# Optimization experiments

Measured on AMD Instinct MI355X. Metric: run time of the kernel, lower is better.

The kernel has to match this reference:

```python
import jax, jax.numpy as jnp
import numpy as np

B, T, C = 4, 2048, 1024
H = 16
D = C // H  # head_dim = 64


def setup_inputs() -> dict:
    key = jax.random.key(0)
    k1, k2, k3 = jax.random.split(key, 3)
    x = jax.random.normal(k1, (B, T, C), dtype=jnp.float32)
    w_qkv = jax.random.normal(k2, (C, 3 * C), dtype=jnp.float32) * (1.0 / np.sqrt(C))
    b_qkv = jnp.zeros((3 * C,), dtype=jnp.float32)
    w_out = jax.random.normal(k3, (C, C), dtype=jnp.float32) * (1.0 / np.sqrt(C))
    b_out = jnp.zeros((C,), dtype=jnp.float32)
    return {"x": x, "w_qkv": w_qkv, "b_qkv": b_qkv, "w_out": w_out, "b_out": b_out}


def reference(x, w_qkv, b_qkv, w_out, b_out):
    # QKV projection: [B,T,3C]
    qkv = x @ w_qkv + b_qkv
    q, k, v = jnp.split(qkv, 3, axis=-1)
    # [B,H,T,D]
    q = q.reshape(B, T, H, D).transpose(0, 2, 1, 3)
    k = k.reshape(B, T, H, D).transpose(0, 2, 1, 3)
    v = v.reshape(B, T, H, D).transpose(0, 2, 1, 3)
    scale = 1.0 / np.sqrt(D)
    # scores: [B,H,T,T]
    scores = jnp.einsum("bhqd,bhkd->bhqk", q, k) * scale
    causal = jnp.tril(jnp.ones((T, T), dtype=bool))
    scores = jnp.where(causal[None, None, :, :], scores, -jnp.inf)
    attn = jax.nn.softmax(scores, axis=-1)
    out = jnp.einsum("bhqk,bhkd->bhqd", attn, v)
    out = out.transpose(0, 2, 1, 3).reshape(B, T, C)
    return out @ w_out + b_out
```

## Files before the change

kernel.cpp:

```cpp
#include <hip/hip_runtime.h>
#include <hip/hip_bf16.h>

#define BB 4
#define TT 2048
#define CC 1024
#define HH 16
#define DD 64

typedef __attribute__((ext_vector_type(8))) short short8;
typedef __attribute__((ext_vector_type(4))) float f32x4;

__device__ __forceinline__ float bf2f(short s) {
  unsigned u = ((unsigned)(unsigned short)s) << 16;
  float f;
  __builtin_memcpy(&f, &u, 4);
  return f;
}
__device__ __forceinline__ short f2bf(float f) {
  unsigned u;
  __builtin_memcpy(&u, &f, 4);
  u = (u + 0x7fffu + ((u >> 16) & 1u)) >> 16;
  return (short)u;
}

__device__ __forceinline__ unsigned cvt_pk_bf16(float lo, float hi) {
  unsigned r;
  asm("v_cvt_pk_bf16_f32 %0, %1, %2" : "=v"(r) : "v"(lo), "v"(hi));
  return r;
}

__device__ __forceinline__ float exp2_fast(float x) {
  float r;
  asm("v_exp_f32 %0, %1" : "=v"(r) : "v"(x));
  return r;
}

template <int CTRL>
__device__ __forceinline__ float dpp_f(float v) {
  union { float f; int i; } u;
  u.f = v;
  u.i = __builtin_amdgcn_update_dpp(0, u.i, CTRL, 0xf, 0xf, true);
  return u.f;
}
__device__ __forceinline__ float rowmax16(float v) {
  v = fmaxf(v, dpp_f<0x128>(v));
  v = fmaxf(v, dpp_f<0x124>(v));
  v = fmaxf(v, dpp_f<0x4E>(v));
  v = fmaxf(v, dpp_f<0xB1>(v));
  return v;
}
__device__ __forceinline__ float rowsum16(float v) {
  v += dpp_f<0x128>(v);
  v += dpp_f<0x124>(v);
  v += dpp_f<0x4E>(v);
  v += dpp_f<0xB1>(v);
  return v;
}

__device__ __forceinline__ void gload_lds16(const void* g, void* l) {
  __builtin_amdgcn_global_load_lds(
      (const __attribute__((address_space(1))) void*)g,
      (__attribute__((address_space(3))) void*)l, 16, 0, 0);
}

__global__ __launch_bounds__(256) void cast_bf16_kernel(
    const float* __restrict__ in, short* __restrict__ out, int n) {
  int i = (blockIdx.x * 256 + threadIdx.x) * 4;
  if (i >= n) return;
  float4 v = *(const float4*)&in[i];
  short4 o;
  o.x = f2bf(v.x); o.y = f2bf(v.y); o.z = f2bf(v.z); o.w = f2bf(v.w);
  *(short4*)&out[i] = o;
}

__global__ __launch_bounds__(256) void transpose_cast_kernel(
    const float* __restrict__ in, short* __restrict__ out, int R, int Cc) {
  __shared__ float tile[32][33];
  const int tx = threadIdx.x, ty = threadIdx.y;
  const int c0 = blockIdx.x * 32, r0 = blockIdx.y * 32;
#pragma unroll
  for (int i = 0; i < 32; i += 8)
    tile[ty + i][tx] = in[(size_t)(r0 + ty + i) * Cc + c0 + tx];
  __syncthreads();
#pragma unroll
  for (int i = 0; i < 32; i += 8)
    out[(size_t)(c0 + ty + i) * R + r0 + tx] = f2bf(tile[tx][ty + i]);
}

template <int MODE>
__global__ __launch_bounds__(256) void gemm_bf16(
    const short* __restrict__ A, const short* __restrict__ Bt,
    const float* __restrict__ bias, float* __restrict__ outF,
    short* __restrict__ outQ, short* __restrict__ outK, short* __restrict__ outV,
    int M, int N, int K) {
  __shared__ __align__(16) short As[128 * 32];
  __shared__ __align__(16) short Bs[128 * 32];
  const int tid = threadIdx.x;
  const int lane = tid & 63, wid = tid >> 6;
  const int wm = wid >> 1, wn = wid & 1;
  const int row0 = blockIdx.y * 128, col0 = blockIdx.x * 128;
  const int fr = lane & 15, fq = lane >> 4;
  const short* Ab = A + (size_t)row0 * K;
  const short* Bb = Bt + (size_t)col0 * K;
  const int sr = tid >> 2;
  const int so = (tid & 3) * 8;

  f32x4 acc[4][4];
#pragma unroll
  for (int m = 0; m < 4; ++m)
#pragma unroll
    for (int n = 0; n < 4; ++n) {
      f32x4 z = {0.f, 0.f, 0.f, 0.f};
      acc[m][n] = z;
    }

  for (int k0 = 0; k0 < K; k0 += 32) {
    __syncthreads();
    gload_lds16(Ab + (size_t)sr * K + k0 + so, &As[tid * 8]);
    gload_lds16(Ab + (size_t)(sr + 64) * K + k0 + so, &As[2048 + tid * 8]);
    gload_lds16(Bb + (size_t)sr * K + k0 + so, &Bs[tid * 8]);
    gload_lds16(Bb + (size_t)(sr + 64) * K + k0 + so, &Bs[2048 + tid * 8]);
    __syncthreads();
    short8 a[4], b[4];
#pragma unroll
    for (int m = 0; m < 4; ++m)
      a[m] = *(const short8*)&As[(wm * 64 + m * 16 + fr) * 32 + fq * 8];
#pragma unroll
    for (int n = 0; n < 4; ++n)
      b[n] = *(const short8*)&Bs[(wn * 64 + n * 16 + fr) * 32 + fq * 8];
#pragma unroll
    for (int m = 0; m < 4; ++m)
#pragma unroll
      for (int n = 0; n < 4; ++n)
        acc[m][n] = __builtin_amdgcn_mfma_f32_16x16x32_bf16(a[m], b[n], acc[m][n], 0, 0, 0);
  }

  float bv[4];
#pragma unroll
  for (int n = 0; n < 4; ++n) bv[n] = bias[col0 + wn * 64 + n * 16 + fr];

  if (MODE == 0) {
#pragma unroll
    for (int m = 0; m < 4; ++m) {
      const int grow = row0 + wm * 64 + m * 16 + fq * 4;
#pragma unroll
      for (int n = 0; n < 4; ++n) {
        const int gcol = col0 + wn * 64 + n * 16 + fr;
#pragma unroll
        for (int r = 0; r < 4; ++r)
          outF[(size_t)(grow + r) * N + gcol] = acc[m][n][r] + bv[n];
      }
    }
  } else {
#pragma unroll
    for (int n = 0; n < 4; ++n) {
      const int gcol = col0 + wn * 64 + n * 16 + fr;
      const int which = gcol >> 10;
      const int h = (gcol & 1023) >> 6;
      const int d = gcol & 63;
      short* dst = (which == 0) ? outQ : (which == 1) ? outK : outV;
#pragma unroll
      for (int m = 0; m < 4; ++m) {
        const int grow = row0 + wm * 64 + m * 16 + fq * 4;
#pragma unroll
        for (int r = 0; r < 4; ++r) {
          const int gb = (grow + r) >> 11;
          const int gt = (grow + r) & 2047;
          const int bh = gb * HH + h;
          size_t idx;
          if (which == 2)
            idx = ((size_t)bh * DD + d) * TT + gt;
          else
            idx = ((size_t)bh * TT + gt) * DD + d;
          dst[idx] = f2bf(acc[m][n][r] + bv[n]);
        }
      }
    }
  }
}

#define C2 0.18033688f

__global__ __launch_bounds__(256) void attn_mfma_kernel(
    const short* __restrict__ q,
    const short* __restrict__ k,
    const short* __restrict__ vt,
    short* __restrict__ ctx) {
  __shared__ __align__(16) short Ks[2][128 * 64];
  __shared__ __align__(16) short Vs[2][64 * 128];
  __shared__ __align__(16) short Ps[4][32 * 64];
  const int tid = threadIdx.x, lane = tid & 63, wid = tid >> 6;
  const int fr = lane & 15, fq = lane >> 4;
  const int lin = blockIdx.x;
  const int bh = lin & 63;
  const int qt = 15 - (lin >> 6);
  const int q0 = qt * 128;
  const int qw0 = q0 + wid * 32;
  const short* kbp = k + (size_t)bh * TT * DD;
  const short* vbp = vt + (size_t)bh * DD * TT;
  char* PsB = (char*)&Ps[wid][0];

#define KSB(c) ((char*)&Ks[0][0] + (c) * (128 * 64 * 2))
#define VSB(c) ((char*)&Vs[0][0] + (c) * (64 * 128 * 2))

  short8 aq[2][2];
#pragma unroll
  for (int m = 0; m < 2; ++m)
#pragma unroll
    for (int ks = 0; ks < 2; ++ks)
      aq[m][ks] = *(const short8*)&q[((size_t)bh * TT + qw0 + m * 16 + fr) * DD + ks * 32 + fq * 8];

  float M[2][4], L[2][4];
  f32x4 o[2][4];
#pragma unroll
  for (int m = 0; m < 2; ++m)
#pragma unroll
    for (int r = 0; r < 4; ++r) { M[m][r] = -1e30f; L[m][r] = 0.f; }
#pragma unroll
  for (int m = 0; m < 2; ++m)
#pragma unroll
    for (int dg = 0; dg < 4; ++dg) {
      f32x4 z = {0.f, 0.f, 0.f, 0.f};
      o[m][dg] = z;
    }

  const int nt = qt + 1;

#define STAGE(c, tt)                                                           \
  do {                                                                         \
    const int kv0_ = (tt) * 128;                                               \
    _Pragma("unroll") for (int b_ = 0; b_ < 4; ++b_) {                         \
      const int lo_ = b_ * 4096 + tid * 16;                                    \
      const int row_ = lo_ >> 7;                                               \
      const int colb_ = lo_ & 127;                                             \
      const int src_ = colb_ ^ ((row_ & 7) << 4);                              \
      gload_lds16(kbp + ((size_t)(kv0_ + row_)) * DD + (src_ >> 1),            \
                  KSB(c) + lo_);                                               \
    }                                                                          \
    _Pragma("unroll") for (int b_ = 0; b_ < 4; ++b_) {                         \
      const int lo_ = b_ * 4096 + tid * 16;                                    \
      const int row_ = lo_ >> 8;                                               \
      const int colb_ = lo_ & 255;                                             \
      const int src_ = colb_ ^ ((row_ & 7) << 4);                              \
      gload_lds16(vbp + (size_t)row_ * TT + kv0_ + (src_ >> 1),                \
                  VSB(c) + lo_);                                               \
    }                                                                          \
  } while (0)

  STAGE(0, 0);

  for (int t = 0; t < nt; ++t) {
    const int cur = t & 1;
    asm volatile("s_waitcnt vmcnt(0)" ::: "memory");
    __builtin_amdgcn_s_barrier();
    if (t + 1 < nt) STAGE(cur ^ 1, t + 1);
    const int kv0 = t * 128;
    if (kv0 > qw0 + 31) continue;

#pragma unroll
    for (int sub = 0; sub < 2; ++sub) {
      const int kv0s = kv0 + sub * 64;
      if (kv0s > qw0 + 31) continue;
      const bool domask = (kv0s + 63 > qw0);

      short8 bk[4][2];
#pragma unroll
      for (int n = 0; n < 4; ++n) {
        const int row = sub * 64 + n * 16 + fr;
#pragma unroll
        for (int ks = 0; ks < 2; ++ks)
          bk[n][ks] = *(const short8*)(KSB(cur) + row * 128 +
                                       (((ks * 64 + fq * 16) ^ ((row & 7) << 4))));
      }
      f32x4 s[2][4];
      __builtin_amdgcn_s_setprio(1);
#pragma unroll
      for (int m = 0; m < 2; ++m)
#pragma unroll
        for (int n = 0; n < 4; ++n) {
          f32x4 z = {0.f, 0.f, 0.f, 0.f};
          s[m][n] = z;
#pragma unroll
          for (int ks = 0; ks < 2; ++ks)
            s[m][n] = __builtin_amdgcn_mfma_f32_16x16x32_bf16(aq[m][ks], bk[n][ks], s[m][n], 0, 0, 0);
        }
      __builtin_amdgcn_s_setprio(0);

      if (domask) {
#pragma unroll
        for (int m = 0; m < 2; ++m)
#pragma unroll
          for (int n = 0; n < 4; ++n)
#pragma unroll
            for (int r = 0; r < 4; ++r) {
              const int qq = qw0 + m * 16 + fq * 4 + r;
              const int kk = kv0s + n * 16 + fr;
              if (kk > qq) s[m][n][r] = -1e30f;
            }
      }

#pragma unroll
      for (int m = 0; m < 2; ++m) {
        float rm2[4];
#pragma unroll
        for (int r = 0; r < 4; ++r) {
          float rm = fmaxf(fmaxf(s[m][0][r], s[m][1][r]), fmaxf(s[m][2][r], s[m][3][r]));
          rm2[r] = rowmax16(rm) * C2;
        }
        float dmax = fmaxf(fmaxf(rm2[0] - M[m][0], rm2[1] - M[m][1]),
                           fmaxf(rm2[2] - M[m][2], rm2[3] - M[m][3]));
        if (__any(dmax > 8.0f)) {
#pragma unroll
          for (int r = 0; r < 4; ++r) {
            const float Mn = fmaxf(M[m][r], rm2[r]);
            const float corr = exp2_fast(M[m][r] - Mn);
            M[m][r] = Mn;
            L[m][r] *= corr;
#pragma unroll
            for (int dg = 0; dg < 4; ++dg) o[m][dg][r] *= corr;
          }
        }
        float psum[4] = {0.f, 0.f, 0.f, 0.f};
        const int brow = m * 16 + fq * 4;
        unsigned short* pw = (unsigned short*)PsB;
#pragma unroll
        for (int n = 0; n < 4; ++n) {
          const float p0 = exp2_fast(__builtin_fmaf(s[m][n][0], C2, -M[m][0]));
          const float p1 = exp2_fast(__builtin_fmaf(s[m][n][1], C2, -M[m][1]));
          const float p2 = exp2_fast(__builtin_fmaf(s[m][n][2], C2, -M[m][2]));
          const float p3 = exp2_fast(__builtin_fmaf(s[m][n][3], C2, -M[m][3]));
          psum[0] += p0; psum[1] += p1; psum[2] += p2; psum[3] += p3;
          const unsigned u0 = cvt_pk_bf16(p0, p1);
          const unsigned u1 = cvt_pk_bf16(p2, p3);
          const int colb = n * 32 + fr * 2;
          pw[((brow + 0) * 128 + (colb ^ (((brow + 0) & 7) << 4))) >> 1] = (unsigned short)u0;
          pw[((brow + 1) * 128 + (colb ^ (((brow + 1) & 7) << 4))) >> 1] = (unsigned short)(u0 >> 16);
          pw[((brow + 2) * 128 + (colb ^ (((brow + 2) & 7) << 4))) >> 1] = (unsigned short)u1;
          pw[((brow + 3) * 128 + (colb ^ (((brow + 3) & 7) << 4))) >> 1] = (unsigned short)(u1 >> 16);
        }
#pragma unroll
        for (int r = 0; r < 4; ++r) L[m][r] += rowsum16(psum[r]);
      }

      short8 ap[2][2], bv[4][2];
#pragma unroll
      for (int m = 0; m < 2; ++m) {
        const int qrow = m * 16 + fr;
#pragma unroll
        for (int ks = 0; ks < 2; ++ks)
          ap[m][ks] = *(const short8*)(PsB + qrow * 128 +
                                       (((ks * 64 + fq * 16) ^ ((qrow & 7) << 4))));
      }
#pragma unroll
      for (int dg = 0; dg < 4; ++dg) {
        const int row = dg * 16 + fr;
#pragma unroll
        for (int ks = 0; ks < 2; ++ks)
          bv[dg][ks] = *(const short8*)(VSB(cur) + row * 256 +
                                        (((sub * 128 + ks * 64 + fq * 16) ^ ((row & 7) << 4))));
      }
      __builtin_amdgcn_s_setprio(1);
#pragma unroll
      for (int m = 0; m < 2; ++m)
#pragma unroll
        for (int dg = 0; dg < 4; ++dg)
#pragma unroll
          for (int ks = 0; ks < 2; ++ks)
            o[m][dg] = __builtin_amdgcn_mfma_f32_16x16x32_bf16(ap[m][ks], bv[dg][ks], o[m][dg], 0, 0, 0);
      __builtin_amdgcn_s_setprio(0);
    }
  }

  const int b = bh >> 4, h = bh & 15;
#pragma unroll
  for (int m = 0; m < 2; ++m)
#pragma unroll
    for (int dg = 0; dg < 4; ++dg)
#pragma unroll
      for (int r = 0; r < 4; ++r) {
        const int qq = qw0 + m * 16 + fq * 4 + r;
        ctx[((size_t)(b * TT + qq)) * CC + h * DD + dg * 16 + fr] =
            f2bf(o[m][dg][r] / L[m][r]);
      }
}

extern "C" void kernel_launch(void* const* d_in, const int* in_sizes, int n_in,
                              void* d_out, int out_size, void* d_ws, size_t ws_size,
                              hipStream_t stream) {
  (void)in_sizes; (void)n_in; (void)out_size; (void)ws_size;
  const float* x = (const float*)d_in[0];
  const float* w_qkv = (const float*)d_in[1];
  const float* b_qkv = (const float*)d_in[2];
  const float* w_out = (const float*)d_in[3];
  const float* b_out = (const float*)d_in[4];
  float* out = (float*)d_out;

  char* w = (char*)d_ws;
  short* xb    = (short*)w; w += (size_t)BB * TT * CC * 2;
  short* wqkvT = (short*)w; w += (size_t)3 * CC * CC * 2;
  short* woutT = (short*)w; w += (size_t)CC * CC * 2;
  short* qb    = (short*)w; w += (size_t)BB * HH * TT * DD * 2;
  short* kb    = (short*)w; w += (size_t)BB * HH * TT * DD * 2;
  short* vtb   = (short*)w; w += (size_t)BB * HH * DD * TT * 2;
  short* ctx   = (short*)w; w += (size_t)BB * TT * CC * 2;

  const int M = BB * TT;

  cast_bf16_kernel<<<dim3((M * CC) / 4 / 256), dim3(256), 0, stream>>>(x, xb, M * CC);
  transpose_cast_kernel<<<dim3(3 * CC / 32, CC / 32), dim3(32, 8), 0, stream>>>(
      w_qkv, wqkvT, CC, 3 * CC);
  transpose_cast_kernel<<<dim3(CC / 32, CC / 32), dim3(32, 8), 0, stream>>>(
      w_out, woutT, CC, CC);

  gemm_bf16<1><<<dim3((3 * CC) / 128, M / 128), dim3(256), 0, stream>>>(
      xb, wqkvT, b_qkv, nullptr, qb, kb, vtb, M, 3 * CC, CC);

  attn_mfma_kernel<<<dim3(16 * 64), dim3(256), 0, stream>>>(qb, kb, vtb, ctx);

  gemm_bf16<0><<<dim3(CC / 128, M / 128), dim3(256), 0, stream>>>(
      ctx, woutT, b_out, out, nullptr, nullptr, nullptr, M, CC, CC);
}
```

Measured before the change: 309.0 us.

## Drop LDS K/V staging; load K and V fragments directly from global per wave

Removes the shared-memory double-buffered K/V staging, its barriers and the block-wide tile loop. Each wave now walks only its own causal range in 64-key steps and loads K and V^T MFMA fragments straight from global memory into registers. This removes block synchronisation and LDS traffic and frees LDS for higher occupancy. In exchange the four waves of a block no longer share K/V reads, so global and L2 traffic rises and load latency is exposed without software pipelining.

```diff
diff --git a/kernel.cpp b/kernel.cpp
--- a/kernel.cpp
+++ b/kernel.cpp
@@ -186,23 +186,17 @@
     const short* __restrict__ k,
     const short* __restrict__ vt,
     short* __restrict__ ctx) {
-  __shared__ __align__(16) short Ks[2][128 * 64];
-  __shared__ __align__(16) short Vs[2][64 * 128];
   __shared__ __align__(16) short Ps[4][32 * 64];
   const int tid = threadIdx.x, lane = tid & 63, wid = tid >> 6;
   const int fr = lane & 15, fq = lane >> 4;
   const int lin = blockIdx.x;
   const int bh = lin & 63;
   const int qt = 15 - (lin >> 6);
-  const int q0 = qt * 128;
-  const int qw0 = q0 + wid * 32;
+  const int qw0 = qt * 128 + wid * 32;
   const short* kbp = k + (size_t)bh * TT * DD;
   const short* vbp = vt + (size_t)bh * DD * TT;
   char* PsB = (char*)&Ps[wid][0];
 
-#define KSB(c) ((char*)&Ks[0][0] + (c) * (128 * 64 * 2))
-#define VSB(c) ((char*)&Vs[0][0] + (c) * (64 * 128 * 2))
-
   short8 aq[2][2];
 #pragma unroll
   for (int m = 0; m < 2; ++m)
@@ -224,151 +218,114 @@
       o[m][dg] = z;
     }
 
-  const int nt = qt + 1;
-
-#define STAGE(c, tt)                                                           \
-  do {                                                                         \
-    const int kv0_ = (tt) * 128;                                               \
-    _Pragma("unroll") for (int b_ = 0; b_ < 4; ++b_) {                         \
-      const int lo_ = b_ * 4096 + tid * 16;                                    \
-      const int row_ = lo_ >> 7;                                               \
-      const int colb_ = lo_ & 127;                                             \
-      const int src_ = colb_ ^ ((row_ & 7) << 4);                              \
-      gload_lds16(kbp + ((size_t)(kv0_ + row_)) * DD + (src_ >> 1),            \
-                  KSB(c) + lo_);                                               \
-    }                                                                          \
-    _Pragma("unroll") for (int b_ = 0; b_ < 4; ++b_) {                         \
-      const int lo_ = b_ * 4096 + tid * 16;                                    \
-      const int row_ = lo_ >> 8;                                               \
-      const int colb_ = lo_ & 255;                                             \
-      const int src_ = colb_ ^ ((row_ & 7) << 4);                              \
-      gload_lds16(vbp + (size_t)row_ * TT + kv0_ + (src_ >> 1),                \
-                  VSB(c) + lo_);                                               \
-    }                                                                          \
-  } while (0)
-
-  STAGE(0, 0);
-
-  for (int t = 0; t < nt; ++t) {
-    const int cur = t & 1;
-    asm volatile("s_waitcnt vmcnt(0)" ::: "memory");
-    __builtin_amdgcn_s_barrier();
-    if (t + 1 < nt) STAGE(cur ^ 1, t + 1);
-    const int kv0 = t * 128;
-    if (kv0 > qw0 + 31) continue;
-
-#pragma unroll
-    for (int sub = 0; sub < 2; ++sub) {
-      const int kv0s = kv0 + sub * 64;
-      if (kv0s > qw0 + 31) continue;
-      const bool domask = (kv0s + 63 > qw0);
-
-      short8 bk[4][2];
+  const int ntw = (qw0 >> 6) + 1;
+
+  for (int t = 0; t < ntw; ++t) {
+    const int kv0s = t * 64;
+    const bool domask = (kv0s + 63 > qw0);
+
+    short8 bk[4][2];
+#pragma unroll
+    for (int n = 0; n < 4; ++n)
+#pragma unroll
+      for (int ks = 0; ks < 2; ++ks)
+        bk[n][ks] = *(const short8*)&kbp[(size_t)(kv0s + n * 16 + fr) * DD + ks * 32 + fq * 8];
+
+    f32x4 s[2][4];
+    __builtin_amdgcn_s_setprio(1);
+#pragma unroll
+    for (int m = 0; m < 2; ++m)
 #pragma unroll
       for (int n = 0; n < 4; ++n) {
-        const int row = sub * 64 + n * 16 + fr;
+        f32x4 z = {0.f, 0.f, 0.f, 0.f};
+        s[m][n] = z;
 #pragma unroll
         for (int ks = 0; ks < 2; ++ks)
-          bk[n][ks] = *(const short8*)(KSB(cur) + row * 128 +
-                                       (((ks * 64 + fq * 16) ^ ((row & 7) << 4))));
-      }
-      f32x4 s[2][4];
-      __builtin_amdgcn_s_setprio(1);
+          s[m][n] = __builtin_amdgcn_mfma_f32_16x16x32_bf16(aq[m][ks], bk[n][ks], s[m][n], 0, 0, 0);
+      }
+    __builtin_amdgcn_s_setprio(0);
+
+    short8 bv[4][2];
+#pragma unroll
+    for (int dg = 0; dg < 4; ++dg)
+#pragma unroll
+      for (int ks = 0; ks < 2; ++ks)
+        bv[dg][ks] = *(const short8*)&vbp[(size_t)(dg * 16 + fr) * TT + kv0s + ks * 32 + fq * 8];
+
+    if (domask) {
 #pragma unroll
       for (int m = 0; m < 2; ++m)
 #pragma unroll
-        for (int n = 0; n < 4; ++n) {
-          f32x4 z = {0.f, 0.f, 0.f, 0.f};
-          s[m][n] = z;
-#pragma unroll
-          for (int ks = 0; ks < 2; ++ks)
-            s[m][n] = __builtin_amdgcn_mfma_f32_16x16x32_bf16(aq[m][ks], bk[n][ks], s[m][n], 0, 0, 0);
+        for (int n = 0; n < 4; ++n)
+#pragma unroll
+          for (int r = 0; r < 4; ++r) {
+            const int qq = qw0 + m * 16 + fq * 4 + r;
+            const int kk = kv0s + n * 16 + fr;
+            if (kk > qq) s[m][n][r] = -1e30f;
+          }
+    }
+
+#pragma unroll
+    for (int m = 0; m < 2; ++m) {
+      float rm2[4];
+#pragma unroll
+      for (int r = 0; r < 4; ++r) {
+        float rm = fmaxf(fmaxf(s[m][0][r], s[m][1][r]), fmaxf(s[m][2][r], s[m][3][r]));
+        rm2[r] = rowmax16(rm) * C2;
+      }
+      float dmax = fmaxf(fmaxf(rm2[0] - M[m][0], rm2[1] - M[m][1]),
+                         fmaxf(rm2[2] - M[m][2], rm2[3] - M[m][3]));
+      if (__any(dmax > 8.0f)) {
+#pragma unroll
+        for (int r = 0; r < 4; ++r) {
+          const float Mn = fmaxf(M[m][r], rm2[r]);
+          const float corr = exp2_fast(M[m][r] - Mn);
+          M[m][r] = Mn;
+          L[m][r] *= corr;
+#pragma unroll
+          for (int dg = 0; dg < 4; ++dg) o[m][dg][r] *= corr;
         }
-      __builtin_amdgcn_s_setprio(0);
-
-      if (domask) {
-#pragma unroll
-        for (int m = 0; m < 2; ++m)
-#pragma unroll
-          for (int n = 0; n < 4; ++n)
-#pragma unroll
-            for (int r = 0; r < 4; ++r) {
-              const int qq = qw0 + m * 16 + fq * 4 + r;
-              const int kk = kv0s + n * 16 + fr;
-              if (kk > qq) s[m][n][r] = -1e30f;
-            }
-      }
-
-#pragma unroll
-      for (int m = 0; m < 2; ++m) {
-        float rm2[4];
-#pragma unroll
-        for (int r = 0; r < 4; ++r) {
-          float rm = fmaxf(fmaxf(s[m][0][r], s[m][1][r]), fmaxf(s[m][2][r], s[m][3][r]));
-          rm2[r] = rowmax16(rm) * C2;
-        }
-        float dmax = fmaxf(fmaxf(rm2[0] - M[m][0], rm2[1] - M[m][1]),
-                           fmaxf(rm2[2] - M[m][2], rm2[3] - M[m][3]));
-        if (__any(dmax > 8.0f)) {
-#pragma unroll
-          for (int r = 0; r < 4; ++r) {
-            const float Mn = fmaxf(M[m][r], rm2[r]);
-            const float corr = exp2_fast(M[m][r] - Mn);
-            M[m][r] = Mn;
-            L[m][r] *= corr;
-#pragma unroll
-            for (int dg = 0; dg < 4; ++dg) o[m][dg][r] *= corr;
-          }
-        }
-        float psum[4] = {0.f, 0.f, 0.f, 0.f};
-        const int brow = m * 16 + fq * 4;
-        unsigned short* pw = (unsigned short*)PsB;
-#pragma unroll
-        for (int n = 0; n < 4; ++n) {
-          const float p0 = exp2_fast(__builtin_fmaf(s[m][n][0], C2, -M[m][0]));
-          const float p1 = exp2_fast(__builtin_fmaf(s[m][n][1], C2, -M[m][1]));
-          const float p2 = exp2_fast(__builtin_fmaf(s[m][n][2], C2, -M[m][2]));
-          const float p3 = exp2_fast(__builtin_fmaf(s[m][n][3], C2, -M[m][3]));
-          psum[0] += p0; psum[1] += p1; psum[2] += p2; psum[3] += p3;
-          const unsigned u0 = cvt_pk_bf16(p0, p1);
-          const unsigned u1 = cvt_pk_bf16(p2, p3);
-          const int colb = n * 32 + fr * 2;
-          pw[((brow + 0) * 128 + (colb ^ (((brow + 0) & 7) << 4))) >> 1] = (unsigned short)u0;
-          pw[((brow + 1) * 128 + (colb ^ (((brow + 1) & 7) << 4))) >> 1] = (unsigned short)(u0 >> 16);
-          pw[((brow + 2) * 128 + (colb ^ (((brow + 2) & 7) << 4))) >> 1] = (unsigned short)u1;
-          pw[((brow + 3) * 128 + (colb ^ (((brow + 3) & 7) << 4))) >> 1] = (unsigned short)(u1 >> 16);
-        }
-#pragma unroll
-        for (int r = 0; r < 4; ++r) L[m][r] += rowsum16(psum[r]);
-      }
-
-      short8 ap[2][2], bv[4][2];
-#pragma unroll
-      for (int m = 0; m < 2; ++m) {
-        const int qrow = m * 16 + fr;
+      }
+      float psum[4] = {0.f, 0.f, 0.f, 0.f};
+      const int brow = m * 16 + fq * 4;
+      unsigned short* pw = (unsigned short*)PsB;
+#pragma unroll
+      for (int n = 0; n < 4; ++n) {
+        const float p0 = exp2_fast(__builtin_fmaf(s[m][n][0], C2, -M[m][0]));
+        const float p1 = exp2_fast(__builtin_fmaf(s[m][n][1], C2, -M[m][1]));
+        const float p2 = exp2_fast(__builtin_fmaf(s[m][n][2], C2, -M[m][2]));
+        const float p3 = exp2_fast(__builtin_fmaf(s[m][n][3], C2, -M[m][3]));
+        psum[0] += p0; psum[1] += p1; psum[2] += p2; psum[3] += p3;
+        const unsigned u0 = cvt_pk_bf16(p0, p1);
+        const unsigned u1 = cvt_pk_bf16(p2, p3);
+        const int colb = n * 32 + fr * 2;
+        pw[((brow + 0) * 128 + (colb ^ (((brow + 0) & 7) << 4))) >> 1] = (unsigned short)u0;
+        pw[((brow + 1) * 128 + (colb ^ (((brow + 1) & 7) << 4))) >> 1] = (unsigned short)(u0 >> 16);
+        pw[((brow + 2) * 128 + (colb ^ (((brow + 2) & 7) << 4))) >> 1] = (unsigned short)u1;
+        pw[((brow + 3) * 128 + (colb ^ (((brow + 3) & 7) << 4))) >> 1] = (unsigned short)(u1 >> 16);
+      }
+#pragma unroll
+      for (int r = 0; r < 4; ++r) L[m][r] += rowsum16(psum[r]);
+    }
+
+    short8 ap[2][2];
+#pragma unroll
+    for (int m = 0; m < 2; ++m) {
+      const int qrow = m * 16 + fr;
+#pragma unroll
+      for (int ks = 0; ks < 2; ++ks)
+        ap[m][ks] = *(const short8*)(PsB + qrow * 128 +
+                                     (((ks * 64 + fq * 16) ^ ((qrow & 7) << 4))));
+    }
+    __builtin_amdgcn_s_setprio(1);
+#pragma unroll
+    for (int m = 0; m < 2; ++m)
+#pragma unroll
+      for (int dg = 0; dg < 4; ++dg)
 #pragma unroll
         for (int ks = 0; ks < 2; ++ks)
-          ap[m][ks] = *(const short8*)(PsB + qrow * 128 +
-                                       (((ks * 64 + fq * 16) ^ ((qrow & 7) << 4))));
-      }
-#pragma unroll
-      for (int dg = 0; dg < 4; ++dg) {
-        const int row = dg * 16 + fr;
-#pragma unroll
-        for (int ks = 0; ks < 2; ++ks)
-          bv[dg][ks] = *(const short8*)(VSB(cur) + row * 256 +
-                                        (((sub * 128 + ks * 64 + fq * 16) ^ ((row & 7) << 4))));
-      }
-      __builtin_amdgcn_s_setprio(1);
-#pragma unroll
-      for (int m = 0; m < 2; ++m)
-#pragma unroll
-        for (int dg = 0; dg < 4; ++dg)
-#pragma unroll
-          for (int ks = 0; ks < 2; ++ks)
-            o[m][dg] = __builtin_amdgcn_mfma_f32_16x16x32_bf16(ap[m][ks], bv[dg][ks], o[m][dg], 0, 0, 0);
-      __builtin_amdgcn_s_setprio(0);
-    }
+          o[m][dg] = __builtin_amdgcn_mfma_f32_16x16x32_bf16(ap[m][ks], bv[dg][ks], o[m][dg], 0, 0, 0);
+    __builtin_amdgcn_s_setprio(0);
   }
 
   const int b = bh >> 4, h = bh & 15;
```

After: 357.9 us. 1.16x slower.
